# Optimization experiments

Measured on AMD Instinct MI355X. Metric: run time of the kernel, lower is better.

## Reference

```python
import jax, jax.numpy as jnp
import numpy as np

B, NE, NR, D1, D2, L = 64, 40000, 500, 200, 200, 64
BN_EPS = 1e-5


def _batchnorm(x, gamma, beta):
    # training-mode BatchNorm1d: biased batch statistics over axis 0
    mu = jnp.mean(x, axis=0)
    var = jnp.var(x, axis=0)
    return gamma * (x - mu) * jax.lax.rsqrt(var + BN_EPS) + beta


def setup_inputs() -> dict:
    key = jax.random.key(0)
    ks = jax.random.split(key, 10)
    return {
        "e1_idx": jax.random.randint(ks[0], (B,), 0, NE),
        "r_idx": jax.random.randint(ks[1], (B,), 0, NR),
        "E": jax.random.normal(ks[2], (NE, D1), dtype=jnp.float32),
        "R": jax.random.normal(ks[3], (NR, D2), dtype=jnp.float32),
        # W ~ Uniform(-1, 1) as in the torch module
        "W": jax.random.uniform(ks[4], (D2, D1, D1), dtype=jnp.float32, minval=-1.0, maxval=1.0),
        # literals normalized into [0, 1]
        "lits": jax.random.uniform(ks[5], (NE, L), dtype=jnp.float32),
        "c": jax.random.normal(ks[6], (L,), dtype=jnp.float32) * 0.1,
        # variance buffer must be positive
        "var_l": jax.random.uniform(ks[7], (L,), dtype=jnp.float32, minval=0.5, maxval=1.5),
        "nf": jax.random.normal(ks[8], (NR, L), dtype=jnp.float32) * 0.1,
        "bn0_gamma": jnp.ones((D1,), jnp.float32),
        "bn0_beta": jnp.zeros((D1,), jnp.float32),
        "bn1_gamma": jnp.ones((D1,), jnp.float32),
        "bn1_beta": jnp.zeros((D1,), jnp.float32),
    }


def reference(e1_idx, r_idx, E, R, W, lits, c, var_l, nf,
              bn0_gamma, bn0_beta, bn1_gamma, bn1_beta):
    # --- TuckER core ---
    e1 = E[e1_idx]                                   # (B, d1)
    x = _batchnorm(e1, bn0_gamma, bn0_beta)          # (B, d1)
    r = R[r_idx]                                     # (B, d2)
    W_mat = jnp.einsum('bk,kij->bij', r, W)          # (B, d1, d1)
    x = jnp.einsum('bi,bij->bj', x, W_mat)           # (B, d1)
    x = _batchnorm(x, bn1_gamma, bn1_beta)
    score_l = x @ E.T                                # (B, N)

    # --- KBLN numeric-literal branch ---
    n_h = lits[e1_idx]                               # (B, L)
    # broadcast instead of .repeat: (B, 1, L) - (1, N, L) -> (B, N, L)
    n = n_h[:, None, :] - lits[None, :, :]
    phi = jnp.exp(-jnp.square(n - c) / var_l)        # (B, N, L)
    w_nf = nf[r_idx]                                 # (B, L)
    score_n = jnp.einsum('bnl,bl->bn', phi, w_nf)    # (B, N)

    return jax.nn.sigmoid(score_l + score_n)
```

## Files before the change

kernel.cpp:

```cpp
#include <hip/hip_runtime.h>
#include <math.h>

#define BB    64
#define NEC   40000
#define NRC   500
#define D1C   200
#define D2C   200
#define LLC   64
#define BN_EPS 1e-5f
#define LOG2E 1.4426950408889634f

#define WS_XT    0
#define WS_RT    12800
#define WS_TAP   25600
#define WS_WP    29696
#define WS_SL    33792
#define WS_X2BH  33856
#define WS_X2BL  42048
#define WS_Y     50240

typedef short s8v __attribute__((ext_vector_type(8)));
typedef float f4v __attribute__((ext_vector_type(4)));

__device__ __forceinline__ unsigned short bf16_rne(float x) {
  unsigned b = __float_as_uint(x);
  unsigned r = b + 0x7FFFu + ((b >> 16) & 1u);
  return (unsigned short)(r >> 16);
}
__device__ __forceinline__ void split2(float x, unsigned short& h,
                                       unsigned short& l) {
  h = bf16_rne(x);
  float hf = __uint_as_float(((unsigned)h) << 16);
  l = bf16_rne(x - hf);
}

typedef __attribute__((address_space(1))) const void gvoid_t;
typedef __attribute__((address_space(3))) void lvoid_t;
__device__ __forceinline__ void gload_lds16(const float* g, float* l) {
  __builtin_amdgcn_global_load_lds((gvoid_t*)g, (lvoid_t*)l, 16, 0, 0);
}

__global__ __launch_bounds__(256) void prep_kernel(
    const int* __restrict__ e1_idx, const int* __restrict__ r_idx,
    const float* __restrict__ E, const float* __restrict__ R,
    const float* __restrict__ lits, const float* __restrict__ c,
    const float* __restrict__ var_l, const float* __restrict__ nf,
    const float* __restrict__ bn0g, const float* __restrict__ bn0b,
    float* __restrict__ ws) {
  float* xT  = ws + WS_XT;
  float* rT  = ws + WS_RT;
  float* taP = ws + WS_TAP;
  float* wP  = ws + WS_WP;
  float* sl  = ws + WS_SL;
  int tid = threadIdx.x;

  if (blockIdx.x == 0) {
    if (tid < D1C) {
      int j = tid;
      float sum = 0.f, sq = 0.f;
      for (int b = 0; b < BB; b++) {
        float e = E[e1_idx[b] * D1C + j];
        sum += e; sq += e * e;
      }
      float mean = sum * (1.f / 64.f);
      float var  = sq  * (1.f / 64.f) - mean * mean;
      float inv  = __builtin_amdgcn_rsqf(var + BN_EPS);
      float g    = bn0g[j] * inv;
      float be   = bn0b[j] - mean * g;
      for (int b = 0; b < BB; b++) {
        xT[j * 64 + b] = g * E[e1_idx[b] * D1C + j] + be;
      }
    }
  } else if (blockIdx.x == 1) {
    for (int idx = tid; idx < D2C * 64; idx += 256) {
      int k = idx >> 6, b = idx & 63;
      rT[idx] = R[r_idx[b] * D2C + k];
    }
  } else if (blockIdx.x == 2) {
    for (int idx = tid; idx < LLC * 64; idx += 256) {
      int l = idx >> 6, b = idx & 63;
      float s = sqrtf(LOG2E / var_l[l]);
      float a = (lits[e1_idx[b] * LLC + l] - c[l]) * s;
      int bp = (b & 15) * 4 + (b >> 4);
      taP[l * 64 + bp] = a + a;
      wP[l * 64 + bp]  = nf[r_idx[b] * LLC + l] * __builtin_amdgcn_exp2f(-a * a);
    }
    if (tid < LLC) sl[tid] = sqrtf(LOG2E / var_l[tid]);
  } else {
    unsigned* z = (unsigned*)(ws + WS_X2BH);
    for (int i = tid; i < 16384; i += 256) z[i] = 0u;
  }
}

#define S1_STAGE(buf_, s_) do {                                         \
    int gbase_ = kbase + (s_) * 8000;                                   \
    _Pragma("unroll")                                                   \
    for (int r_ = 0; r_ < 4; r_++) {                                    \
      int off_ = r_ * 2048 + w * 256;                                   \
      int gi_ = gbase_ + off_ + lane4;                                  \
      gi_ = gi_ < 7999996 ? gi_ : 7999996;                              \
      gload_lds16(W + gi_, &Wb[buf_][off_]);                            \
    }                                                                   \
  } while (0)

__global__ __launch_bounds__(512) void stage1_kernel(
    const float* __restrict__ W, const float* __restrict__ ws_in,
    float* __restrict__ y) {
  const float* xT = ws_in + WS_XT;
  const float* rT = ws_in + WS_RT;
  __shared__ float Wb[2][8192];

  int k = blockIdx.x;
  int tid = threadIdx.x;
  int lane = tid & 63;
  int w = __builtin_amdgcn_readfirstlane(tid >> 6);
  int jc = w & 3, bh = w >> 2;
  int j4 = lane & 15, bq = lane >> 4;
  int j0 = jc * 64 + j4 * 4;
  int b0 = bh * 32 + bq * 8;
  bool jok = j0 < 200;
  int joff = jok ? j0 : 0;
  int kbase = k * 40000;
  int lane4 = lane * 4;

  float acc[4][8];
#pragma unroll
  for (int jj = 0; jj < 4; jj++)
#pragma unroll
    for (int bb = 0; bb < 8; bb++) acc[jj][bb] = 0.f;

  S1_STAGE(0, 0);
  for (int s = 0; s < 5; s++) {
    __syncthreads();
    if (s < 4) S1_STAGE((s + 1) & 1, s + 1);
    const float* Ws = Wb[s & 1];
    const float* xrow = xT + s * 40 * 64 + b0;
#pragma unroll 4
    for (int ri = 0; ri < 40; ri++) {
      float4 wv  = *(const float4*)(Ws + ri * 200 + joff);
      float4 xa  = *(const float4*)(xrow + ri * 64);
      float4 xb2 = *(const float4*)(xrow + ri * 64 + 4);
      float wc[4] = {wv.x, wv.y, wv.z, wv.w};
      float xv[8] = {xa.x, xa.y, xa.z, xa.w, xb2.x, xb2.y, xb2.z, xb2.w};
#pragma unroll
      for (int jj = 0; jj < 4; jj++)
#pragma unroll
        for (int bb = 0; bb < 8; bb++)
          acc[jj][bb] += wc[jj] * xv[bb];
    }
  }

  if (jok) {
    float4 r0 = *(const float4*)(rT + k * 64 + b0);
    float4 r1 = *(const float4*)(rT + k * 64 + b0 + 4);
    float rv[8] = {r0.x, r0.y, r0.z, r0.w, r1.x, r1.y, r1.z, r1.w};
#pragma unroll
    for (int jj = 0; jj < 4; jj++) {
      float* yo = y + (k * D1C + j0 + jj) * 64 + b0;
      float4 o0 = make_float4(acc[jj][0] * rv[0], acc[jj][1] * rv[1],
                              acc[jj][2] * rv[2], acc[jj][3] * rv[3]);
      float4 o1 = make_float4(acc[jj][4] * rv[4], acc[jj][5] * rv[5],
                              acc[jj][6] * rv[6], acc[jj][7] * rv[7]);
      *(float4*)(yo) = o0;
      *(float4*)(yo + 4) = o1;
    }
  }
}

__global__ __launch_bounds__(256) void reduce_bn1_kernel(
    const float* __restrict__ y, const float* __restrict__ bn1g,
    const float* __restrict__ bn1b, float* __restrict__ ws) {
  int j = blockIdx.x;
  int tid = threadIdx.x, b = tid & 63, kq = tid >> 6;

  float s = 0.f;
  const float* yp = y + (kq * 50 * D1C + j) * 64 + b;
  for (int k = 0; k < 50; k++) s += yp[k * D1C * 64];

  __shared__ float part[256];
  part[tid] = s;
  __syncthreads();
  if (tid < 64) {
    float v = part[tid] + part[64 + tid] + part[128 + tid] + part[192 + tid];
    float sum = v, sq = v * v;
#pragma unroll
    for (int o = 32; o > 0; o >>= 1) {
      sum += __shfl_xor(sum, o, 64);
      sq  += __shfl_xor(sq,  o, 64);
    }
    float mean = sum * (1.f / 64.f);
    float var  = sq  * (1.f / 64.f) - mean * mean;
    float inv  = __builtin_amdgcn_rsqf(var + BN_EPS);
    float g    = bn1g[j] * inv;
    float be   = bn1b[j] - mean * g;
    float xv   = g * v + be;
    unsigned short h, l;
    split2(xv, h, l);
    unsigned short* xh = (unsigned short*)(ws + WS_X2BH);
    unsigned short* xl = (unsigned short*)(ws + WS_X2BL);
    xh[tid * 256 + j] = h;
    xl[tid * 256 + j] = l;
  }
}

__global__ __launch_bounds__(256, 2) void final_kernel(
    const float* __restrict__ E, const float* __restrict__ lits,
    const float* __restrict__ ws, float* __restrict__ out) {
  const float* taP = ws + WS_TAP;
  const float* wP  = ws + WS_WP;
  const float* sl  = ws + WS_SL;
  const unsigned short* x2bh = (const unsigned short*)(ws + WS_X2BH);
  const unsigned short* x2bl = (const unsigned short*)(ws + WS_X2BL);

  __shared__ float SM[9216];
  unsigned short* Ah = (unsigned short*)SM;
  unsigned short* Al = Ah + 4608;
  unsigned short* Bh = Ah + 9216;
  unsigned short* Bl = Ah + 13824;

  int n0 = blockIdx.x * 64;
  int tid = threadIdx.x;
  int lane = tid & 63;
  int w = __builtin_amdgcn_readfirstlane(tid >> 6);
  int ln = lane & 15;
  int quad = lane >> 4;

  f4v acc[4];
#pragma unroll
  for (int t = 0; t < 4; t++) acc[t] = (f4v){0.f, 0.f, 0.f, 0.f};

  for (int q = 0; q < 4; q++) {
    int k0 = q * 64;
    __syncthreads();
#pragma unroll
    for (int it = 0; it < 4; it++) {
      int idx = tid + it * 256;
      int row = idx >> 4, c4 = idx & 15, cc = c4 * 4;
      float4 v = make_float4(0.f, 0.f, 0.f, 0.f);
      if (k0 + cc < 200) v = *(const float4*)(E + (n0 + row) * D1C + k0 + cc);
      unsigned short h0, l0, h1, l1, h2, l2, h3, l3;
      split2(v.x, h0, l0); split2(v.y, h1, l1);
      split2(v.z, h2, l2); split2(v.w, h3, l3);
      *(ushort4*)(Ah + row * 72 + cc) = make_ushort4(h0, h1, h2, h3);
      *(ushort4*)(Al + row * 72 + cc) = make_ushort4(l0, l1, l2, l3);
    }
#pragma unroll
    for (int it = 0; it < 4; it++) {
      int idx = tid + it * 256;
      int row = idx >> 4, c4 = idx & 15;
      *(ushort4*)(Bh + row * 72 + c4 * 4) =
          *(const ushort4*)(x2bh + row * 256 + k0 + c4 * 4);
      *(ushort4*)(Bl + row * 72 + c4 * 4) =
          *(const ushort4*)(x2bl + row * 256 + k0 + c4 * 4);
    }
    __syncthreads();

    const unsigned short* Ab  = Ah + (16 * w + ln) * 72 + quad * 8;
    const unsigned short* Alb = Al + (16 * w + ln) * 72 + quad * 8;
#pragma unroll
    for (int ks = 0; ks < 64; ks += 32) {
      s8v ah = *(const s8v*)(Ab + ks);
      s8v al = *(const s8v*)(Alb + ks);
#pragma unroll
      for (int t = 0; t < 4; t++) {
        s8v bh = *(const s8v*)(Bh + (16 * t + ln) * 72 + quad * 8 + ks);
        s8v bl = *(const s8v*)(Bl + (16 * t + ln) * 72 + quad * 8 + ks);
        acc[t] = __builtin_amdgcn_mfma_f32_16x16x32_bf16(ah, bh, acc[t], 0, 0, 0);
        acc[t] = __builtin_amdgcn_mfma_f32_16x16x32_bf16(al, bh, acc[t], 0, 0, 0);
        acc[t] = __builtin_amdgcn_mfma_f32_16x16x32_bf16(ah, bl, acc[t], 0, 0, 0);
      }
    }
  }

  float* Llds = SM;
  float* TAl  = SM + 4352;
  float* Wl   = SM + 6400;
  int nlb = 16 * w + 4 * quad;

  __syncthreads();
#pragma unroll
  for (int it = 0; it < 4; it++) {
    int idx = tid + it * 256;
    int row = idx >> 4, c4 = idx & 15;
    float4 v = *(const float4*)(lits + (n0 + row) * LLC + c4 * 4);
    int l = c4 * 4;
    Llds[(l + 0) * 68 + row] = v.x * sl[l + 0];
    Llds[(l + 1) * 68 + row] = v.y * sl[l + 1];
    Llds[(l + 2) * 68 + row] = v.z * sl[l + 2];
    Llds[(l + 3) * 68 + row] = v.w * sl[l + 3];
  }

  for (int h = 0; h < 2; h++) {
    __syncthreads();
#pragma unroll
    for (int it = 0; it < 2; it++) {
      int idx = tid + it * 256;
      ((float4*)TAl)[idx] = ((const float4*)(taP + h * 2048))[idx];
      ((float4*)Wl)[idx]  = ((const float4*)(wP  + h * 2048))[idx];
    }
    __syncthreads();
    for (int ll = 0; ll < 32; ll++) {
      float4 Lv = *(const float4*)(Llds + (h * 32 + ll) * 68 + nlb);
      float4 ta = *(const float4*)(TAl + ll * 64 + 4 * ln);
      float4 wv = *(const float4*)(Wl  + ll * 64 + 4 * ln);
      float Lc[4]  = {Lv.x, Lv.y, Lv.z, Lv.w};
      float tac[4] = {ta.x, ta.y, ta.z, ta.w};
      float wvc[4] = {wv.x, wv.y, wv.z, wv.w};
      float n2[4];
#pragma unroll
      for (int r = 0; r < 4; r++) n2[r] = -Lc[r] * Lc[r];
#pragma unroll
      for (int t = 0; t < 4; t++) {
#pragma unroll
        for (int r = 0; r < 4; r++) {
          acc[t][r] += wvc[t] *
              __builtin_amdgcn_exp2f(__builtin_fmaf(tac[t], Lc[r], n2[r]));
        }
      }
    }
  }

#pragma unroll
  for (int t = 0; t < 4; t++) {
    float4 o;
    o.x = __builtin_amdgcn_rcpf(1.f + __builtin_amdgcn_exp2f(-LOG2E * acc[t][0]));
    o.y = __builtin_amdgcn_rcpf(1.f + __builtin_amdgcn_exp2f(-LOG2E * acc[t][1]));
    o.z = __builtin_amdgcn_rcpf(1.f + __builtin_amdgcn_exp2f(-LOG2E * acc[t][2]));
    o.w = __builtin_amdgcn_rcpf(1.f + __builtin_amdgcn_exp2f(-LOG2E * acc[t][3]));
    *(float4*)(out + (size_t)(16 * t + ln) * NEC + n0 + nlb) = o;
  }
}

extern "C" void kernel_launch(void* const* d_in, const int* in_sizes, int n_in,
                              void* d_out, int out_size, void* d_ws, size_t ws_size,
                              hipStream_t stream) {
  (void)in_sizes; (void)n_in; (void)out_size; (void)ws_size;
  const int*   e1    = (const int*)d_in[0];
  const int*   ri    = (const int*)d_in[1];
  const float* E     = (const float*)d_in[2];
  const float* R     = (const float*)d_in[3];
  const float* W     = (const float*)d_in[4];
  const float* lits  = (const float*)d_in[5];
  const float* c     = (const float*)d_in[6];
  const float* var_l = (const float*)d_in[7];
  const float* nf    = (const float*)d_in[8];
  const float* bn0g  = (const float*)d_in[9];
  const float* bn0b  = (const float*)d_in[10];
  const float* bn1g  = (const float*)d_in[11];
  const float* bn1b  = (const float*)d_in[12];
  float* out = (float*)d_out;
  float* ws  = (float*)d_ws;
  float* y   = ws + WS_Y;

  prep_kernel<<<4, 256, 0, stream>>>(e1, ri, E, R, lits, c, var_l, nf,
                                     bn0g, bn0b, ws);
  stage1_kernel<<<200, 512, 0, stream>>>(W, ws, y);
  reduce_bn1_kernel<<<200, 256, 0, stream>>>(y, bn1g, bn1b, ws);
  final_kernel<<<625, 256, 0, stream>>>(E, lits, ws, out);
}
```

Baseline: 199.2 us.

## Load MFMA operands directly from global memory instead of staging through LDS

```diff
diff --git a/kernel.cpp b/kernel.cpp
--- a/kernel.cpp
+++ b/kernel.cpp
@@ -203,7 +203,7 @@
   }
 }
 
-__global__ __launch_bounds__(256, 2) void final_kernel(
+__global__ __launch_bounds__(256, 3) void final_kernel(
     const float* __restrict__ E, const float* __restrict__ lits,
     const float* __restrict__ ws, float* __restrict__ out) {
   const float* taP = ws + WS_TAP;
@@ -212,11 +212,7 @@
   const unsigned short* x2bh = (const unsigned short*)(ws + WS_X2BH);
   const unsigned short* x2bl = (const unsigned short*)(ws + WS_X2BL);
 
-  __shared__ float SM[9216];
-  unsigned short* Ah = (unsigned short*)SM;
-  unsigned short* Al = Ah + 4608;
-  unsigned short* Bh = Ah + 9216;
-  unsigned short* Bl = Ah + 13824;
+  __shared__ float Llds[64 * 68];
 
   int n0 = blockIdx.x * 64;
   int tid = threadIdx.x;
@@ -225,59 +221,6 @@
   int ln = lane & 15;
   int quad = lane >> 4;
 
-  f4v acc[4];
-#pragma unroll
-  for (int t = 0; t < 4; t++) acc[t] = (f4v){0.f, 0.f, 0.f, 0.f};
-
-  for (int q = 0; q < 4; q++) {
-    int k0 = q * 64;
-    __syncthreads();
-#pragma unroll
-    for (int it = 0; it < 4; it++) {
-      int idx = tid + it * 256;
-      int row = idx >> 4, c4 = idx & 15, cc = c4 * 4;
-      float4 v = make_float4(0.f, 0.f, 0.f, 0.f);
-      if (k0 + cc < 200) v = *(const float4*)(E + (n0 + row) * D1C + k0 + cc);
-      unsigned short h0, l0, h1, l1, h2, l2, h3, l3;
-      split2(v.x, h0, l0); split2(v.y, h1, l1);
-      split2(v.z, h2, l2); split2(v.w, h3, l3);
-      *(ushort4*)(Ah + row * 72 + cc) = make_ushort4(h0, h1, h2, h3);
-      *(ushort4*)(Al + row * 72 + cc) = make_ushort4(l0, l1, l2, l3);
-    }
-#pragma unroll
-    for (int it = 0; it < 4; it++) {
-      int idx = tid + it * 256;
-      int row = idx >> 4, c4 = idx & 15;
-      *(ushort4*)(Bh + row * 72 + c4 * 4) =
-          *(const ushort4*)(x2bh + row * 256 + k0 + c4 * 4);
-      *(ushort4*)(Bl + row * 72 + c4 * 4) =
-          *(const ushort4*)(x2bl + row * 256 + k0 + c4 * 4);
-    }
-    __syncthreads();
-
-    const unsigned short* Ab  = Ah + (16 * w + ln) * 72 + quad * 8;
-    const unsigned short* Alb = Al + (16 * w + ln) * 72 + quad * 8;
-#pragma unroll
-    for (int ks = 0; ks < 64; ks += 32) {
-      s8v ah = *(const s8v*)(Ab + ks);
-      s8v al = *(const s8v*)(Alb + ks);
-#pragma unroll
-      for (int t = 0; t < 4; t++) {
-        s8v bh = *(const s8v*)(Bh + (16 * t + ln) * 72 + quad * 8 + ks);
-        s8v bl = *(const s8v*)(Bl + (16 * t + ln) * 72 + quad * 8 + ks);
-        acc[t] = __builtin_amdgcn_mfma_f32_16x16x32_bf16(ah, bh, acc[t], 0, 0, 0);
-        acc[t] = __builtin_amdgcn_mfma_f32_16x16x32_bf16(al, bh, acc[t], 0, 0, 0);
-        acc[t] = __builtin_amdgcn_mfma_f32_16x16x32_bf16(ah, bl, acc[t], 0, 0, 0);
-      }
-    }
-  }
-
-  float* Llds = SM;
-  float* TAl  = SM + 4352;
-  float* Wl   = SM + 6400;
-  int nlb = 16 * w + 4 * quad;
-
-  __syncthreads();
 #pragma unroll
   for (int it = 0; it < 4; it++) {
     int idx = tid + it * 256;
@@ -290,32 +233,69 @@
     Llds[(l + 3) * 68 + row] = v.w * sl[l + 3];
   }
 
-  for (int h = 0; h < 2; h++) {
-    __syncthreads();
-#pragma unroll
-    for (int it = 0; it < 2; it++) {
-      int idx = tid + it * 256;
-      ((float4*)TAl)[idx] = ((const float4*)(taP + h * 2048))[idx];
-      ((float4*)Wl)[idx]  = ((const float4*)(wP  + h * 2048))[idx];
-    }
-    __syncthreads();
-    for (int ll = 0; ll < 32; ll++) {
-      float4 Lv = *(const float4*)(Llds + (h * 32 + ll) * 68 + nlb);
-      float4 ta = *(const float4*)(TAl + ll * 64 + 4 * ln);
-      float4 wv = *(const float4*)(Wl  + ll * 64 + 4 * ln);
-      float Lc[4]  = {Lv.x, Lv.y, Lv.z, Lv.w};
-      float tac[4] = {ta.x, ta.y, ta.z, ta.w};
-      float wvc[4] = {wv.x, wv.y, wv.z, wv.w};
-      float n2[4];
-#pragma unroll
-      for (int r = 0; r < 4; r++) n2[r] = -Lc[r] * Lc[r];
-#pragma unroll
-      for (int t = 0; t < 4; t++) {
-#pragma unroll
-        for (int r = 0; r < 4; r++) {
-          acc[t][r] += wvc[t] *
-              __builtin_amdgcn_exp2f(__builtin_fmaf(tac[t], Lc[r], n2[r]));
-        }
+  f4v acc[4];
+#pragma unroll
+  for (int t = 0; t < 4; t++) acc[t] = (f4v){0.f, 0.f, 0.f, 0.f};
+
+  int arow = n0 + 16 * w + ln;
+  const float* Ea = E + arow * D1C + quad * 8;
+
+  float4 av[12];
+#pragma unroll
+  for (int ks = 0; ks < 6; ks++) {
+    av[2 * ks]     = *(const float4*)(Ea + ks * 32);
+    av[2 * ks + 1] = *(const float4*)(Ea + ks * 32 + 4);
+  }
+  float4 at0 = make_float4(0.f, 0.f, 0.f, 0.f), at1 = at0;
+  if (quad == 0) {
+    at0 = *(const float4*)(Ea + 192);
+    at1 = *(const float4*)(Ea + 196);
+  }
+
+#pragma unroll
+  for (int ks = 0; ks < 7; ks++) {
+    float4 va = (ks < 6) ? av[2 * ks]     : at0;
+    float4 vb = (ks < 6) ? av[2 * ks + 1] : at1;
+    float f[8] = {va.x, va.y, va.z, va.w, vb.x, vb.y, vb.z, vb.w};
+    s8v ah, al;
+#pragma unroll
+    for (int e = 0; e < 8; e++) {
+      unsigned short hh, ll;
+      split2(f[e], hh, ll);
+      ah[e] = (short)hh;
+      al[e] = (short)ll;
+    }
+    int kb = quad * 8 + ks * 32;
+#pragma unroll
+    for (int t = 0; t < 4; t++) {
+      s8v bh = *(const s8v*)(x2bh + (16 * t + ln) * 256 + kb);
+      s8v bl = *(const s8v*)(x2bl + (16 * t + ln) * 256 + kb);
+      acc[t] = __builtin_amdgcn_mfma_f32_16x16x32_bf16(ah, bh, acc[t], 0, 0, 0);
+      acc[t] = __builtin_amdgcn_mfma_f32_16x16x32_bf16(al, bh, acc[t], 0, 0, 0);
+      acc[t] = __builtin_amdgcn_mfma_f32_16x16x32_bf16(ah, bl, acc[t], 0, 0, 0);
+    }
+  }
+
+  __syncthreads();
+  int nlb = 16 * w + 4 * quad;
+
+#pragma unroll 2
+  for (int ll = 0; ll < 64; ll++) {
+    float4 Lv = *(const float4*)(&Llds[ll * 68 + nlb]);
+    float4 ta = *(const float4*)(taP + ll * 64 + 4 * ln);
+    float4 wv = *(const float4*)(wP  + ll * 64 + 4 * ln);
+    float Lc[4]  = {Lv.x, Lv.y, Lv.z, Lv.w};
+    float tac[4] = {ta.x, ta.y, ta.z, ta.w};
+    float wvc[4] = {wv.x, wv.y, wv.z, wv.w};
+    float n2[4];
+#pragma unroll
+    for (int r = 0; r < 4; r++) n2[r] = -Lc[r] * Lc[r];
+#pragma unroll
+    for (int t = 0; t < 4; t++) {
+#pragma unroll
+      for (int r = 0; r < 4; r++) {
+        acc[t][r] += wvc[t] *
+            __builtin_amdgcn_exp2f(__builtin_fmaf(tac[t], Lc[r], n2[r]));
       }
     }
   }
```

Result: slower. 209.9 us (+5.3%).

## Split final kernel across 8 waves and coalesce prep gathers

Applied to the files above, without the earlier changes.

```diff
diff --git a/kernel.cpp b/kernel.cpp
--- a/kernel.cpp
+++ b/kernel.cpp
@@ -53,32 +53,46 @@
   float* wP  = ws + WS_WP;
   float* sl  = ws + WS_SL;
   int tid = threadIdx.x;
+  int lane = tid & 63;
+  int wv = tid >> 6;
 
   if (blockIdx.x == 0) {
+    __shared__ float tile[64][201];
+    __shared__ float gA[200], bA[200];
+    for (int b = wv; b < 64; b += 4) {
+      const float* src = E + e1_idx[b] * D1C;
+      for (int j = lane; j < D1C; j += 64) tile[b][j] = src[j];
+    }
+    __syncthreads();
     if (tid < D1C) {
       int j = tid;
       float sum = 0.f, sq = 0.f;
       for (int b = 0; b < BB; b++) {
-        float e = E[e1_idx[b] * D1C + j];
+        float e = tile[b][j];
         sum += e; sq += e * e;
       }
       float mean = sum * (1.f / 64.f);
       float var  = sq  * (1.f / 64.f) - mean * mean;
       float inv  = __builtin_amdgcn_rsqf(var + BN_EPS);
       float g    = bn0g[j] * inv;
-      float be   = bn0b[j] - mean * g;
-      for (int b = 0; b < BB; b++) {
-        xT[j * 64 + b] = g * E[e1_idx[b] * D1C + j] + be;
-      }
+      gA[j] = g;
+      bA[j] = bn0b[j] - mean * g;
+    }
+    __syncthreads();
+    for (int idx = tid; idx < 64 * D1C; idx += 256) {
+      int j = idx >> 6, b = idx & 63;
+      xT[idx] = gA[j] * tile[b][j] + bA[j];
     }
   } else if (blockIdx.x == 1) {
-    for (int idx = tid; idx < D2C * 64; idx += 256) {
-      int k = idx >> 6, b = idx & 63;
-      rT[idx] = R[r_idx[b] * D2C + k];
+    for (int b = wv; b < 64; b += 4) {
+      const float* src = R + r_idx[b] * D2C;
+      for (int k = lane; k < D2C; k += 64) rT[k * 64 + b] = src[k];
     }
   } else if (blockIdx.x == 2) {
-    for (int idx = tid; idx < LLC * 64; idx += 256) {
-      int l = idx >> 6, b = idx & 63;
+#pragma unroll 4
+    for (int it = 0; it < 16; it++) {
+      int idx = tid + it * 256;
+      int b = idx >> 6, l = idx & 63;
       float s = sqrtf(LOG2E / var_l[l]);
       float a = (lits[e1_idx[b] * LLC + l] - c[l]) * s;
       int bp = (b & 15) * 4 + (b >> 4);
@@ -203,7 +217,7 @@
   }
 }
 
-__global__ __launch_bounds__(256, 2) void final_kernel(
+__global__ __launch_bounds__(512, 4) void final_kernel(
     const float* __restrict__ E, const float* __restrict__ lits,
     const float* __restrict__ ws, float* __restrict__ out) {
   const float* taP = ws + WS_TAP;
@@ -212,7 +226,7 @@
   const unsigned short* x2bh = (const unsigned short*)(ws + WS_X2BH);
   const unsigned short* x2bl = (const unsigned short*)(ws + WS_X2BL);
 
-  __shared__ float SM[9216];
+  __shared__ float SM[12608];
   unsigned short* Ah = (unsigned short*)SM;
   unsigned short* Al = Ah + 4608;
   unsigned short* Bh = Ah + 9216;
@@ -222,19 +236,21 @@
   int tid = threadIdx.x;
   int lane = tid & 63;
   int w = __builtin_amdgcn_readfirstlane(tid >> 6);
+  int nc = w & 3;
+  int bh2 = (w >> 2) * 2;
   int ln = lane & 15;
   int quad = lane >> 4;
 
-  f4v acc[4];
-#pragma unroll
-  for (int t = 0; t < 4; t++) acc[t] = (f4v){0.f, 0.f, 0.f, 0.f};
+  f4v acc[2];
+#pragma unroll
+  for (int t = 0; t < 2; t++) acc[t] = (f4v){0.f, 0.f, 0.f, 0.f};
 
   for (int q = 0; q < 4; q++) {
     int k0 = q * 64;
     __syncthreads();
 #pragma unroll
-    for (int it = 0; it < 4; it++) {
-      int idx = tid + it * 256;
+    for (int it = 0; it < 2; it++) {
+      int idx = tid + it * 512;
       int row = idx >> 4, c4 = idx & 15, cc = c4 * 4;
       float4 v = make_float4(0.f, 0.f, 0.f, 0.f);
       if (k0 + cc < 200) v = *(const float4*)(E + (n0 + row) * D1C + k0 + cc);
@@ -245,8 +261,8 @@
       *(ushort4*)(Al + row * 72 + cc) = make_ushort4(l0, l1, l2, l3);
     }
 #pragma unroll
-    for (int it = 0; it < 4; it++) {
-      int idx = tid + it * 256;
+    for (int it = 0; it < 2; it++) {
+      int idx = tid + it * 512;
       int row = idx >> 4, c4 = idx & 15;
       *(ushort4*)(Bh + row * 72 + c4 * 4) =
           *(const ushort4*)(x2bh + row * 256 + k0 + c4 * 4);
@@ -255,78 +271,73 @@
     }
     __syncthreads();
 
-    const unsigned short* Ab  = Ah + (16 * w + ln) * 72 + quad * 8;
-    const unsigned short* Alb = Al + (16 * w + ln) * 72 + quad * 8;
+    const unsigned short* Ab  = Ah + (16 * nc + ln) * 72 + quad * 8;
+    const unsigned short* Alb = Al + (16 * nc + ln) * 72 + quad * 8;
 #pragma unroll
     for (int ks = 0; ks < 64; ks += 32) {
       s8v ah = *(const s8v*)(Ab + ks);
       s8v al = *(const s8v*)(Alb + ks);
 #pragma unroll
-      for (int t = 0; t < 4; t++) {
+      for (int tt = 0; tt < 2; tt++) {
+        int t = bh2 + tt;
         s8v bh = *(const s8v*)(Bh + (16 * t + ln) * 72 + quad * 8 + ks);
         s8v bl = *(const s8v*)(Bl + (16 * t + ln) * 72 + quad * 8 + ks);
-        acc[t] = __builtin_amdgcn_mfma_f32_16x16x32_bf16(ah, bh, acc[t], 0, 0, 0);
-        acc[t] = __builtin_amdgcn_mfma_f32_16x16x32_bf16(al, bh, acc[t], 0, 0, 0);
-        acc[t] = __builtin_amdgcn_mfma_f32_16x16x32_bf16(ah, bl, acc[t], 0, 0, 0);
+        acc[tt] = __builtin_amdgcn_mfma_f32_16x16x32_bf16(ah, bh, acc[tt], 0, 0, 0);
+        acc[tt] = __builtin_amdgcn_mfma_f32_16x16x32_bf16(al, bh, acc[tt], 0, 0, 0);
+        acc[tt] = __builtin_amdgcn_mfma_f32_16x16x32_bf16(ah, bl, acc[tt], 0, 0, 0);
       }
     }
   }
 
   float* Llds = SM;
-  float* TAl  = SM + 4352;
-  float* Wl   = SM + 6400;
-  int nlb = 16 * w + 4 * quad;
-
+  float* TA   = SM + 4416;
+  float* WV   = SM + 8512;
   __syncthreads();
 #pragma unroll
-  for (int it = 0; it < 4; it++) {
-    int idx = tid + it * 256;
+  for (int it = 0; it < 2; it++) {
+    int idx = tid + it * 512;
     int row = idx >> 4, c4 = idx & 15;
     float4 v = *(const float4*)(lits + (n0 + row) * LLC + c4 * 4);
     int l = c4 * 4;
-    Llds[(l + 0) * 68 + row] = v.x * sl[l + 0];
-    Llds[(l + 1) * 68 + row] = v.y * sl[l + 1];
-    Llds[(l + 2) * 68 + row] = v.z * sl[l + 2];
-    Llds[(l + 3) * 68 + row] = v.w * sl[l + 3];
-  }
-
-  for (int h = 0; h < 2; h++) {
-    __syncthreads();
-#pragma unroll
-    for (int it = 0; it < 2; it++) {
-      int idx = tid + it * 256;
-      ((float4*)TAl)[idx] = ((const float4*)(taP + h * 2048))[idx];
-      ((float4*)Wl)[idx]  = ((const float4*)(wP  + h * 2048))[idx];
-    }
-    __syncthreads();
-    for (int ll = 0; ll < 32; ll++) {
-      float4 Lv = *(const float4*)(Llds + (h * 32 + ll) * 68 + nlb);
-      float4 ta = *(const float4*)(TAl + ll * 64 + 4 * ln);
-      float4 wv = *(const float4*)(Wl  + ll * 64 + 4 * ln);
-      float Lc[4]  = {Lv.x, Lv.y, Lv.z, Lv.w};
-      float tac[4] = {ta.x, ta.y, ta.z, ta.w};
-      float wvc[4] = {wv.x, wv.y, wv.z, wv.w};
-      float n2[4];
-#pragma unroll
-      for (int r = 0; r < 4; r++) n2[r] = -Lc[r] * Lc[r];
-#pragma unroll
-      for (int t = 0; t < 4; t++) {
-#pragma unroll
-        for (int r = 0; r < 4; r++) {
-          acc[t][r] += wvc[t] *
-              __builtin_amdgcn_exp2f(__builtin_fmaf(tac[t], Lc[r], n2[r]));
-        }
+    Llds[(l + 0) * 69 + row] = v.x * sl[l + 0];
+    Llds[(l + 1) * 69 + row] = v.y * sl[l + 1];
+    Llds[(l + 2) * 69 + row] = v.z * sl[l + 2];
+    Llds[(l + 3) * 69 + row] = v.w * sl[l + 3];
+    ((float4*)TA)[idx] = ((const float4*)taP)[idx];
+    ((float4*)WV)[idx] = ((const float4*)wP)[idx];
+  }
+  __syncthreads();
+
+  int nlb = 16 * nc + 4 * quad;
+#pragma unroll 2
+  for (int ll = 0; ll < 64; ll++) {
+    float4 Lv = *(const float4*)(&Llds[ll * 69 + nlb]);
+    float2 ta = *(const float2*)(TA + ll * 64 + 4 * ln + bh2);
+    float2 wv = *(const float2*)(WV + ll * 64 + 4 * ln + bh2);
+    float Lc[4]  = {Lv.x, Lv.y, Lv.z, Lv.w};
+    float tac[2] = {ta.x, ta.y};
+    float wvc[2] = {wv.x, wv.y};
+    float n2[4];
+#pragma unroll
+    for (int r = 0; r < 4; r++) n2[r] = -Lc[r] * Lc[r];
+#pragma unroll
+    for (int tt = 0; tt < 2; tt++) {
+#pragma unroll
+      for (int r = 0; r < 4; r++) {
+        acc[tt][r] += wvc[tt] *
+            __builtin_amdgcn_exp2f(__builtin_fmaf(tac[tt], Lc[r], n2[r]));
       }
     }
   }
 
 #pragma unroll
-  for (int t = 0; t < 4; t++) {
+  for (int tt = 0; tt < 2; tt++) {
+    int t = bh2 + tt;
     float4 o;
-    o.x = __builtin_amdgcn_rcpf(1.f + __builtin_amdgcn_exp2f(-LOG2E * acc[t][0]));
-    o.y = __builtin_amdgcn_rcpf(1.f + __builtin_amdgcn_exp2f(-LOG2E * acc[t][1]));
-    o.z = __builtin_amdgcn_rcpf(1.f + __builtin_amdgcn_exp2f(-LOG2E * acc[t][2]));
-    o.w = __builtin_amdgcn_rcpf(1.f + __builtin_amdgcn_exp2f(-LOG2E * acc[t][3]));
+    o.x = __builtin_amdgcn_rcpf(1.f + __builtin_amdgcn_exp2f(-LOG2E * acc[tt][0]));
+    o.y = __builtin_amdgcn_rcpf(1.f + __builtin_amdgcn_exp2f(-LOG2E * acc[tt][1]));
+    o.z = __builtin_amdgcn_rcpf(1.f + __builtin_amdgcn_exp2f(-LOG2E * acc[tt][2]));
+    o.w = __builtin_amdgcn_rcpf(1.f + __builtin_amdgcn_exp2f(-LOG2E * acc[tt][3]));
     *(float4*)(out + (size_t)(16 * t + ln) * NEC + n0 + nlb) = o;
   }
 }
@@ -356,5 +367,5 @@
                                      bn0g, bn0b, ws);
   stage1_kernel<<<200, 512, 0, stream>>>(W, ws, y);
   reduce_bn1_kernel<<<200, 256, 0, stream>>>(y, bn1g, bn1b, ws);
-  final_kernel<<<625, 256, 0, stream>>>(E, lits, ws, out);
-}
+  final_kernel<<<625, 512, 0, stream>>>(E, lits, ws, out);
+}
```

Measured after the change: 236.1 us. +18.5%, slower.
